# Kernel tuning notes

Hardware: AMD Instinct MI355X
Metric: run time of the kernel (lower is better)

Reference implementation:

```python
import jax, jax.numpy as jnp
import numpy as np

B, T, N = 16, 1024, 512

def setup_inputs() -> dict:
    key = jax.random.key(0)
    ks = jax.random.split(key, 6)
    scale = 1.0 / np.sqrt(N)
    x = jax.random.normal(ks[0], (B, T, N), dtype=jnp.float32)
    Wq = jax.random.normal(ks[1], (N, N), dtype=jnp.float32) * scale
    Wk = jax.random.normal(ks[2], (N, N), dtype=jnp.float32) * scale
    Wv = jax.random.normal(ks[3], (N, N), dtype=jnp.float32) * scale
    Wp = jax.random.normal(ks[4], (N, N), dtype=jnp.float32) * scale
    bp = jnp.zeros((N,), dtype=jnp.float32)
    return {"x": x, "Wq": Wq, "Wk": Wk, "Wv": Wv, "Wp": Wp, "bp": bp}

def reference(x, Wq, Wk, Wv, Wp, bp):
    # x: [B, T, N]; conv1d(k=1) over node channels == 'oi,bit->bot' on x^T [B,N,T]
    xt = jnp.swapaxes(x, -1, -2)                     # [B, N, T]
    q = jnp.einsum('oi,bit->bot', Wq, xt)            # [B, N, T]
    k = jnp.einsum('oi,bit->bot', Wk, xt)
    v = jnp.einsum('oi,bit->bot', Wv, xt)
    n = x.shape[-1]
    attn = jnp.einsum('bnt,bmt->bnm', q, k) * (n ** -0.5)  # [B, N, N]
    attn = jax.nn.softmax(attn, axis=-1)
    px = jnp.einsum('bnm,bmt->bnt', attn, v)         # [B, N, T]
    px = jnp.swapaxes(px, -1, -2)                    # [B, T, N]
    out = jnp.einsum('btn,on->bto', px, Wp) + bp     # Linear(N,N)
    return out
```

## Files before the change

### kernel.cpp

```cpp
#include <hip/hip_runtime.h>
#include <stdint.h>

#define BB 16
#define TT 1024
#define NN 512

typedef unsigned short u16;
typedef __bf16 bf16_t;
typedef bf16_t bf16x8 __attribute__((ext_vector_type(8)));
typedef float f32x4 __attribute__((ext_vector_type(4)));

struct alignas(8) U16x4 { u16 x, y, z, w; };
struct alignas(16) F32x4 { float x, y, z, w; };

__device__ __forceinline__ u16 f2bf(float f) {
    union { float f; uint32_t u; } v; v.f = f;
    uint32_t r = v.u + 0x7fffu + ((v.u >> 16) & 1u);
    return (u16)(r >> 16);
}

__device__ __forceinline__ void gload_lds16(const void* g, void* l) {
    __builtin_amdgcn_global_load_lds(
        (const __attribute__((address_space(1))) void*)g,
        (__attribute__((address_space(3))) void*)l, 16, 0, 0);
}

__device__ __forceinline__ void xcd_swizzle(int gx, int gy, int& bx, int& by) {
    const int nwg  = gx * gy;
    const int orig = by * gx + bx;
    const int q = nwg >> 3, r = nwg & 7;
    const int xcd = orig & 7, loc = orig >> 3;
    const int swz = (xcd < r ? xcd * (q + 1) : r * (q + 1) + (xcd - r) * q) + loc;
    bx = swz % gx;
    by = swz / gx;
}

__global__ __launch_bounds__(256)
void cvt_all(const float* __restrict__ x,
             const float* __restrict__ Wq, const float* __restrict__ Wk,
             const float* __restrict__ Wv, const float* __restrict__ Wp,
             u16* __restrict__ xb, u16* __restrict__ wb) {
    int c = blockIdx.x * 256 + threadIdx.x;
    const float* src;
    u16* dst;
    int idx;
    if (c < 2097152) {
        src = x; dst = xb; idx = c;
    } else {
        c -= 2097152;
        const int w = c >> 16;
        idx = c & 65535;
        src = (w == 0) ? Wq : (w == 1) ? Wk : (w == 2) ? Wv : Wp;
        dst = wb + (w << 18);
        idx += 0;
        dst = wb; idx = (w << 16) + (c & 65535);
    }
    F32x4 f = ((const F32x4*)src)[ (src == x) ? idx : (idx & 65535) ];
    U16x4 u;
    u.x = f2bf(f.x); u.y = f2bf(f.y); u.z = f2bf(f.z); u.w = f2bf(f.w);
    ((U16x4*)dst)[idx] = u;
}

template<int MODE, int SPLITK>
__global__ __launch_bounds__(256)
void gemm_nt(const u16* __restrict__ Ag, const u16* __restrict__ Bg,
             void* __restrict__ Cg, const float* __restrict__ bias,
             int M, int Nc, int K, int lda, int ldb,
             long sA, long sB, long sC)
{
    int zb = blockIdx.z, kof = 0;
    if (SPLITK) { kof = (zb >> 4) * K; zb &= 15; }
    const u16* A  = Ag + (long)zb * sA + kof;
    const u16* Bt = Bg + (long)zb * sB + kof;

    __shared__ u16 As[2][4096];
    __shared__ u16 Bs[2][4096];

    int bx = blockIdx.x, by = blockIdx.y;
    xcd_swizzle(gridDim.x, gridDim.y, bx, by);

    const int tid  = threadIdx.x;
    const int wave = tid >> 6;
    const int lane = tid & 63;
    const int arow0 = by * 128;
    const int brow0 = bx * 128;
    const int wr = (wave >> 1) * 64;
    const int wc = (wave & 1) * 64;

    const int srow  = tid >> 2;
    const int sf    = ((srow >> 1) & 3) << 4;
    const int gcol  = ((tid & 3) << 4) ^ sf;
    const char* Asrc = (const char*)A  + (long)(arow0 + srow) * lda * 2 + gcol;
    const char* Bsrc = (const char*)Bt + (long)(brow0 + srow) * ldb * 2 + gcol;
    const long rstepA = (long)64 * lda * 2;
    const long rstepB = (long)64 * ldb * 2;

    f32x4 zero = {0.f, 0.f, 0.f, 0.f};
    f32x4 acc[4][4];
#pragma unroll
    for (int i = 0; i < 4; i++)
#pragma unroll
        for (int j = 0; j < 4; j++) acc[i][j] = zero;

    const int kTiles = K >> 5;

    auto stage = [&](int buf, int kt) {
        const long kb = (long)kt * 64;
        char* ad = (char*)As + buf * 8192 + tid * 16;
        char* bd = (char*)Bs + buf * 8192 + tid * 16;
        gload_lds16(Asrc + kb,          ad);
        gload_lds16(Bsrc + kb,          bd);
        gload_lds16(Asrc + rstepA + kb, ad + 4096);
        gload_lds16(Bsrc + rstepB + kb, bd + 4096);
    };

    stage(0, 0);
    int cur = 0;
    const int kbyte = (lane >> 4) << 4;
    const int rA = lane & 15;

    for (int kt = 0; kt < kTiles; ++kt) {
        if (kt + 1 < kTiles) {
            stage(cur ^ 1, kt + 1);
            asm volatile("s_waitcnt vmcnt(4)" ::: "memory");
        } else {
            asm volatile("s_waitcnt vmcnt(0)" ::: "memory");
        }
        __builtin_amdgcn_s_barrier();
        asm volatile("" ::: "memory");

        bf16x8 av[4], bv[4];
        const char* as = (const char*)As + cur * 8192;
        const char* bs = (const char*)Bs + cur * 8192;
#pragma unroll
        for (int m = 0; m < 4; m++) {
            const int row = wr + m * 16 + rA;
            av[m] = *(const bf16x8*)(as + row * 64 + (kbyte ^ (((row >> 1) & 3) << 4)));
        }
#pragma unroll
        for (int n = 0; n < 4; n++) {
            const int row = wc + n * 16 + rA;
            bv[n] = *(const bf16x8*)(bs + row * 64 + (kbyte ^ (((row >> 1) & 3) << 4)));
        }
#pragma unroll
        for (int m = 0; m < 4; m++)
#pragma unroll
            for (int n = 0; n < 4; n++)
                acc[m][n] = __builtin_amdgcn_mfma_f32_16x16x32_bf16(av[m], bv[n], acc[m][n], 0, 0, 0);

        asm volatile("" ::: "memory");
        __builtin_amdgcn_s_barrier();
        cur ^= 1;
    }

    const int r0 = (lane >> 4) << 2;
    const int cl = lane & 15;
#pragma unroll
    for (int m = 0; m < 4; m++) {
        const long gm = (long)arow0 + wr + m * 16 + r0;
#pragma unroll
        for (int n = 0; n < 4; n++) {
            const long gn = (long)brow0 + wc + n * 16 + cl;
            if (MODE == 0) {
                u16* O = (u16*)Cg + blockIdx.z * sC;
#pragma unroll
                for (int r = 0; r < 4; r++)
                    O[(gm + r) * Nc + gn] = f2bf(acc[m][n][r]);
            } else if (MODE == 4) {
                const long b = gm >> 10;
                const long t = gm & 1023;
                if (gn < 1024) {
                    u16* O = (u16*)Cg + (gn >> 9) * ((long)BB * NN * TT);
                    const long col = gn & 511;
                    U16x4 u;
                    u.x = f2bf(acc[m][n][0]); u.y = f2bf(acc[m][n][1]);
                    u.z = f2bf(acc[m][n][2]); u.w = f2bf(acc[m][n][3]);
                    *(U16x4*)(O + (b * 512 + col) * 1024 + t) = u;
                } else {
                    u16* V = (u16*)Cg + 2L * BB * NN * TT;
                    const int vc = (int)gn - 1024;
#pragma unroll
                    for (int r = 0; r < 4; r++)
                        V[(gm + r) * NN + vc] = f2bf(acc[m][n][r]);
                }
            } else {
                float* O = (float*)Cg + blockIdx.z * sC;
                const float bb = (MODE == 3) ? bias[gn] : 0.f;
#pragma unroll
                for (int r = 0; r < 4; r++)
                    O[(gm + r) * Nc + gn] = acc[m][n][r] + bb;
            }
        }
    }
}

__global__ __launch_bounds__(256)
void softmax_rows(float* __restrict__ S0, const float* __restrict__ S1)
{
    const long r = blockIdx.x;
    float* row0 = S0 + r * 512;
    const float* row1 = S1 + r * 512;
    const int t = threadIdx.x;
    const int lane = t & 63, wave = t >> 6;
    const float scale = 0.04419417382415922f;

    float a = (row0[t]       + row1[t])       * scale;
    float b = (row0[t + 256] + row1[t + 256]) * scale;

    float m = fmaxf(a, b);
#pragma unroll
    for (int o = 32; o; o >>= 1) m = fmaxf(m, __shfl_xor(m, o, 64));

    __shared__ float red[8];
    if (lane == 0) red[wave] = m;
    __syncthreads();
    m = fmaxf(fmaxf(red[0], red[1]), fmaxf(red[2], red[3]));

    float e0 = __expf(a - m), e1 = __expf(b - m);
    float s = e0 + e1;
#pragma unroll
    for (int o = 32; o; o >>= 1) s += __shfl_xor(s, o, 64);
    if (lane == 0) red[wave + 4] = s;
    __syncthreads();
    s = red[4] + red[5] + red[6] + red[7];
    const float inv = 1.f / s;

    u16* P = (u16*)row0;
    P[t]       = f2bf(e0 * inv);
    P[t + 256] = f2bf(e1 * inv);
}

extern "C" void kernel_launch(void* const* d_in, const int* in_sizes, int n_in,
                              void* d_out, int out_size, void* d_ws, size_t ws_size,
                              hipStream_t stream)
{
    (void)in_sizes; (void)n_in; (void)out_size; (void)ws_size;
    const float* x  = (const float*)d_in[0];
    const float* Wq = (const float*)d_in[1];
    const float* Wk = (const float*)d_in[2];
    const float* Wv = (const float*)d_in[3];
    const float* Wp = (const float*)d_in[4];
    const float* bp = (const float*)d_in[5];
    float* out = (float*)d_out;

    char* ws = (char*)d_ws;
    size_t o = 0;
    auto alloc = [&](size_t bytes) {
        char* p = ws + o;
        o = (o + bytes + 255) & ~(size_t)255;
        return p;
    };
    u16* xb  = (u16*)alloc((size_t)BB * TT * NN * 2);
    u16* wb  = (u16*)alloc((size_t)4 * NN * NN * 2);
    u16* qkv = (u16*)alloc((size_t)3 * BB * NN * TT * 2);
    float* S = (float*)alloc((size_t)2 * BB * NN * NN * 4);
    u16* px  = xb;

    const u16* qb  = qkv;
    const u16* kbp = qkv + (size_t)BB * NN * TT;
    const u16* vb  = qkv + (size_t)2 * BB * NN * TT;
    const u16* wpb = wb + (size_t)3 * NN * NN;
    float* S1 = S + (size_t)BB * NN * NN;

    cvt_all<<<dim3(9216), dim3(256), 0, stream>>>(x, Wq, Wk, Wv, Wp, xb, wb);

    const dim3 blk(256);

    const dim3 gq(12, 128, 1);
    gemm_nt<4, 0><<<gq, blk, 0, stream>>>(xb, wb, qkv, nullptr,
                                          BB * TT, 1536, NN, NN, NN, 0, 0, 0);

    const dim3 g2(NN / 128, NN / 128, 2 * BB);
    gemm_nt<2, 1><<<g2, blk, 0, stream>>>(qb, kbp, S, nullptr, NN, NN, TT / 2, TT, TT,
                                          (long)NN * TT, (long)NN * TT, (long)NN * NN);

    softmax_rows<<<dim3(BB * NN), dim3(256), 0, stream>>>(S, S1);

    const dim3 g3(NN / 128, TT / 128, BB);
    gemm_nt<0, 0><<<g3, blk, 0, stream>>>(vb, (const u16*)S, px, nullptr, TT, NN, NN, NN, 1024,
                                          (long)TT * NN, (long)NN * 1024, (long)TT * NN);

    const dim3 g1(NN / 128, (BB * TT) / 128, 1);
    gemm_nt<3, 0><<<g1, blk, 0, stream>>>(px, wpb, out, bp, BB * TT, NN, NN, NN, NN, 0, 0, 0);
}
```

Before: 195.2 us.

## Reassociate attention via Gram matrix x^T x to avoid materializing Q, K, V

```diff
diff --git a/kernel.cpp b/kernel.cpp
--- a/kernel.cpp
+++ b/kernel.cpp
@@ -36,42 +36,87 @@
 }
 
 __global__ __launch_bounds__(256)
-void cvt_all(const float* __restrict__ x,
-             const float* __restrict__ Wq, const float* __restrict__ Wk,
-             const float* __restrict__ Wv, const float* __restrict__ Wp,
-             u16* __restrict__ xb, u16* __restrict__ wb) {
-    int c = blockIdx.x * 256 + threadIdx.x;
-    const float* src;
-    u16* dst;
-    int idx;
-    if (c < 2097152) {
-        src = x; dst = xb; idx = c;
+void cvt_x(const float* __restrict__ x, u16* __restrict__ xb, u16* __restrict__ xT)
+{
+    __shared__ u16 tile[64][70];
+    const int b  = blockIdx.z;
+    const int t0 = blockIdx.x * 64;
+    const int n0 = blockIdx.y * 64;
+    const int i  = threadIdx.x;
+#pragma unroll
+    for (int rep = 0; rep < 4; rep++) {
+        const int lin = rep * 256 + i;
+        const int r = lin >> 4, c4 = (lin & 15) * 4;
+        const long src = ((long)(b * TT + t0 + r)) * NN + n0 + c4;
+        F32x4 f = *(const F32x4*)&x[src];
+        U16x4 u;
+        u.x = f2bf(f.x); u.y = f2bf(f.y); u.z = f2bf(f.z); u.w = f2bf(f.w);
+        *(U16x4*)&xb[src] = u;
+        tile[r][c4] = u.x; tile[r][c4 + 1] = u.y; tile[r][c4 + 2] = u.z; tile[r][c4 + 3] = u.w;
+    }
+    __syncthreads();
+#pragma unroll
+    for (int rep = 0; rep < 4; rep++) {
+        const int lin = rep * 256 + i;
+        const int n = lin >> 4, t4 = (lin & 15) * 4;
+        U16x4 u;
+        u.x = tile[t4][n]; u.y = tile[t4 + 1][n]; u.z = tile[t4 + 2][n]; u.w = tile[t4 + 3][n];
+        *(U16x4*)&xT[((long)(b * NN + n0 + n)) * TT + t0 + t4] = u;
+    }
+}
+
+__global__ __launch_bounds__(256)
+void cvt_w(const float* __restrict__ Wq, const float* __restrict__ Wk,
+           const float* __restrict__ Wv, const float* __restrict__ Wp,
+           u16* __restrict__ wb)
+{
+    __shared__ u16 tile[64][70];
+    const int z  = blockIdx.z;
+    const int r0 = blockIdx.x * 64;
+    const int c0 = blockIdx.y * 64;
+    const int i  = threadIdx.x;
+    const float* src = (z == 0) ? Wq : (z == 1) ? Wk : (z == 2) ? Wv : Wp;
+    u16* dst = wb + z * 262144;
+    if (z != 2) {
+#pragma unroll
+        for (int rep = 0; rep < 4; rep++) {
+            const int lin = rep * 256 + i;
+            const int r = lin >> 4, c4 = (lin & 15) * 4;
+            F32x4 f = *(const F32x4*)&src[(r0 + r) * 512 + c0 + c4];
+            U16x4 u;
+            u.x = f2bf(f.x); u.y = f2bf(f.y); u.z = f2bf(f.z); u.w = f2bf(f.w);
+            *(U16x4*)&dst[(r0 + r) * 512 + c0 + c4] = u;
+        }
     } else {
-        c -= 2097152;
-        const int w = c >> 16;
-        idx = c & 65535;
-        src = (w == 0) ? Wq : (w == 1) ? Wk : (w == 2) ? Wv : Wp;
-        dst = wb + (w << 18);
-        idx += 0;
-        dst = wb; idx = (w << 16) + (c & 65535);
-    }
-    F32x4 f = ((const F32x4*)src)[ (src == x) ? idx : (idx & 65535) ];
-    U16x4 u;
-    u.x = f2bf(f.x); u.y = f2bf(f.y); u.z = f2bf(f.z); u.w = f2bf(f.w);
-    ((U16x4*)dst)[idx] = u;
-}
-
-template<int MODE, int SPLITK>
+#pragma unroll
+        for (int rep = 0; rep < 4; rep++) {
+            const int lin = rep * 256 + i;
+            const int r = lin >> 4, c4 = (lin & 15) * 4;
+            F32x4 f = *(const F32x4*)&src[(r0 + r) * 512 + c0 + c4];
+            tile[r][c4]     = f2bf(f.x); tile[r][c4 + 1] = f2bf(f.y);
+            tile[r][c4 + 2] = f2bf(f.z); tile[r][c4 + 3] = f2bf(f.w);
+        }
+        __syncthreads();
+#pragma unroll
+        for (int rep = 0; rep < 4; rep++) {
+            const int lin = rep * 256 + i;
+            const int n = lin >> 4, t4 = (lin & 15) * 4;
+            U16x4 u;
+            u.x = tile[t4][n]; u.y = tile[t4 + 1][n]; u.z = tile[t4 + 2][n]; u.w = tile[t4 + 3][n];
+            *(U16x4*)&dst[(c0 + n) * 512 + r0 + t4] = u;
+        }
+    }
+}
+
+template<int MODE>
 __global__ __launch_bounds__(256)
 void gemm_nt(const u16* __restrict__ Ag, const u16* __restrict__ Bg,
              void* __restrict__ Cg, const float* __restrict__ bias,
-             int M, int Nc, int K, int lda, int ldb,
+             int Nc, int K, int lda, int ldb,
              long sA, long sB, long sC)
 {
-    int zb = blockIdx.z, kof = 0;
-    if (SPLITK) { kof = (zb >> 4) * K; zb &= 15; }
-    const u16* A  = Ag + (long)zb * sA + kof;
-    const u16* Bt = Bg + (long)zb * sB + kof;
+    const u16* A  = Ag + (long)blockIdx.z * sA;
+    const u16* Bt = Bg + (long)blockIdx.z * sB;
 
     __shared__ u16 As[2][4096];
     __shared__ u16 Bs[2][4096];
@@ -87,9 +132,9 @@
     const int wr = (wave >> 1) * 64;
     const int wc = (wave & 1) * 64;
 
-    const int srow  = tid >> 2;
-    const int sf    = ((srow >> 1) & 3) << 4;
-    const int gcol  = ((tid & 3) << 4) ^ sf;
+    const int srow = tid >> 2;
+    const int sf   = ((srow >> 1) & 3) << 4;
+    const int gcol = ((tid & 3) << 4) ^ sf;
     const char* Asrc = (const char*)A  + (long)(arow0 + srow) * lda * 2 + gcol;
     const char* Bsrc = (const char*)Bt + (long)(brow0 + srow) * ldb * 2 + gcol;
     const long rstepA = (long)64 * lda * 2;
@@ -166,23 +211,6 @@
 #pragma unroll
                 for (int r = 0; r < 4; r++)
                     O[(gm + r) * Nc + gn] = f2bf(acc[m][n][r]);
-            } else if (MODE == 4) {
-                const long b = gm >> 10;
-                const long t = gm & 1023;
-                if (gn < 1024) {
-                    u16* O = (u16*)Cg + (gn >> 9) * ((long)BB * NN * TT);
-                    const long col = gn & 511;
-                    U16x4 u;
-                    u.x = f2bf(acc[m][n][0]); u.y = f2bf(acc[m][n][1]);
-                    u.z = f2bf(acc[m][n][2]); u.w = f2bf(acc[m][n][3]);
-                    *(U16x4*)(O + (b * 512 + col) * 1024 + t) = u;
-                } else {
-                    u16* V = (u16*)Cg + 2L * BB * NN * TT;
-                    const int vc = (int)gn - 1024;
-#pragma unroll
-                    for (int r = 0; r < 4; r++)
-                        V[(gm + r) * NN + vc] = f2bf(acc[m][n][r]);
-                }
             } else {
                 float* O = (float*)Cg + blockIdx.z * sC;
                 const float bb = (MODE == 3) ? bias[gn] : 0.f;
@@ -195,17 +223,16 @@
 }
 
 __global__ __launch_bounds__(256)
-void softmax_rows(float* __restrict__ S0, const float* __restrict__ S1)
+void softmax_rows(float* __restrict__ S)
 {
     const long r = blockIdx.x;
-    float* row0 = S0 + r * 512;
-    const float* row1 = S1 + r * 512;
+    float* row = S + r * 512;
     const int t = threadIdx.x;
     const int lane = t & 63, wave = t >> 6;
     const float scale = 0.04419417382415922f;
 
-    float a = (row0[t]       + row1[t])       * scale;
-    float b = (row0[t + 256] + row1[t + 256]) * scale;
+    float a = row[t] * scale;
+    float b = row[t + 256] * scale;
 
     float m = fmaxf(a, b);
 #pragma unroll
@@ -225,7 +252,7 @@
     s = red[4] + red[5] + red[6] + red[7];
     const float inv = 1.f / s;
 
-    u16* P = (u16*)row0;
+    u16* P = (u16*)row;
     P[t]       = f2bf(e0 * inv);
     P[t + 256] = f2bf(e1 * inv);
 }
@@ -250,36 +277,43 @@
         o = (o + bytes + 255) & ~(size_t)255;
         return p;
     };
-    u16* xb  = (u16*)alloc((size_t)BB * TT * NN * 2);
-    u16* wb  = (u16*)alloc((size_t)4 * NN * NN * 2);
-    u16* qkv = (u16*)alloc((size_t)3 * BB * NN * TT * 2);
-    float* S = (float*)alloc((size_t)2 * BB * NN * NN * 4);
-    u16* px  = xb;
-
-    const u16* qb  = qkv;
-    const u16* kbp = qkv + (size_t)BB * NN * TT;
-    const u16* vb  = qkv + (size_t)2 * BB * NN * TT;
-    const u16* wpb = wb + (size_t)3 * NN * NN;
-    float* S1 = S + (size_t)BB * NN * NN;
-
-    cvt_all<<<dim3(9216), dim3(256), 0, stream>>>(x, Wq, Wk, Wv, Wp, xb, wb);
+    u16* xb = (u16*)alloc((size_t)BB * TT * NN * 2);
+    u16* xT = (u16*)alloc((size_t)BB * NN * TT * 2);
+    u16* wb = (u16*)alloc((size_t)4 * NN * NN * 2);
+    u16* G  = (u16*)alloc((size_t)BB * NN * NN * 2);
+    u16* H  = (u16*)alloc((size_t)BB * NN * NN * 2);
+    float* S = (float*)alloc((size_t)BB * NN * NN * 4);
+    u16* R  = (u16*)alloc((size_t)BB * NN * NN * 2);
+    u16* px = (u16*)alloc((size_t)BB * TT * NN * 2);
+
+    const u16* wqb  = wb;
+    const u16* wkb  = wb + 1 * 262144;
+    const u16* wvtb = wb + 2 * 262144;
+    const u16* wpb  = wb + 3 * 262144;
+    const long NSQ = (long)NN * NN;
+
+    cvt_x<<<dim3(16, 8, 16), dim3(256), 0, stream>>>(x, xb, xT);
+    cvt_w<<<dim3(8, 8, 4),  dim3(256), 0, stream>>>(Wq, Wk, Wv, Wp, wb);
 
     const dim3 blk(256);
 
-    const dim3 gq(12, 128, 1);
-    gemm_nt<4, 0><<<gq, blk, 0, stream>>>(xb, wb, qkv, nullptr,
-                                          BB * TT, 1536, NN, NN, NN, 0, 0, 0);
-
-    const dim3 g2(NN / 128, NN / 128, 2 * BB);
-    gemm_nt<2, 1><<<g2, blk, 0, stream>>>(qb, kbp, S, nullptr, NN, NN, TT / 2, TT, TT,
-                                          (long)NN * TT, (long)NN * TT, (long)NN * NN);
-
-    softmax_rows<<<dim3(BB * NN), dim3(256), 0, stream>>>(S, S1);
-
-    const dim3 g3(NN / 128, TT / 128, BB);
-    gemm_nt<0, 0><<<g3, blk, 0, stream>>>(vb, (const u16*)S, px, nullptr, TT, NN, NN, NN, 1024,
-                                          (long)TT * NN, (long)NN * 1024, (long)TT * NN);
-
-    const dim3 g1(NN / 128, (BB * TT) / 128, 1);
-    gemm_nt<3, 0><<<g1, blk, 0, stream>>>(px, wpb, out, bp, BB * TT, NN, NN, NN, NN, 0, 0, 0);
-}
+    gemm_nt<0><<<dim3(4, 4, 16), blk, 0, stream>>>(xT, xT, G, nullptr,
+        NN, TT, TT, TT, (long)NN * TT, (long)NN * TT, NSQ);
+
+    gemm_nt<0><<<dim3(4, 4, 16), blk, 0, stream>>>(wqb, G, H, nullptr,
+        NN, NN, NN, NN, 0, NSQ, NSQ);
+
+    gemm_nt<2><<<dim3(4, 4, 16), blk, 0, stream>>>(H, wkb, S, nullptr,
+        NN, NN, NN, NN, NSQ, 0, NSQ);
+
+    softmax_rows<<<dim3(BB * NN), blk, 0, stream>>>(S);
+
+    gemm_nt<0><<<dim3(4, 4, 16), blk, 0, stream>>>((const u16*)S, wvtb, R, nullptr,
+        NN, NN, 1024, NN, (long)NN * 1024, 0, NSQ);
+
+    gemm_nt<0><<<dim3(4, 8, 16), blk, 0, stream>>>(xb, R, px, nullptr,
+        NN, NN, NN, NN, (long)TT * NN, NSQ, (long)TT * NN);
+
+    gemm_nt<3><<<dim3(4, 128, 1), blk, 0, stream>>>(px, wpb, out, bp,
+        NN, NN, NN, NN, 0, 0, 0);
+}
```

Result: slower. 199.4 us (+2.1%).
